# Kernel optimization log

Hardware: AMD Instinct MI355X
Metric: run time of the kernel (lower is better)

## Reference

```python
import jax, jax.numpy as jnp
import numpy as np

EMBED_DIM = 1024
NUM_HEADS = 16
HEAD_DIM = EMBED_DIM // NUM_HEADS


def setup_inputs() -> dict:
    key = jax.random.key(0)
    ks = jax.random.split(key, 9)
    B, T, C = 4, 2048, EMBED_DIM
    s = 1.0 / np.sqrt(C)
    return {
        "x": jax.random.normal(ks[0], (B, T, C), jnp.float32),
        "Wq": jax.random.normal(ks[1], (C, C), jnp.float32) * s,
        "bq": jnp.zeros((C,), jnp.float32),
        "Wk": jax.random.normal(ks[2], (C, C), jnp.float32) * s,
        "bk": jnp.zeros((C,), jnp.float32),
        "Wv": jax.random.normal(ks[3], (C, C), jnp.float32) * s,
        "bv": jnp.zeros((C,), jnp.float32),
        "Wo": jax.random.normal(ks[4], (C, C), jnp.float32) * s,
        "bo": jnp.zeros((C,), jnp.float32),
    }


def reference(x, Wq, bq, Wk, bk, Wv, bv, Wo, bo):
    B, T, C = x.shape
    H, D = NUM_HEADS, HEAD_DIM
    # projections (torch Linear: y = x @ W.T + b; here weights stored as [in, out])
    q = (x @ Wq + bq).reshape(B, T, H, D).transpose(0, 2, 1, 3)  # [B,H,T,D]
    k = (x @ Wk + bk).reshape(B, T, H, D).transpose(0, 2, 1, 3)
    v = (x @ Wv + bv).reshape(B, T, H, D).transpose(0, 2, 1, 3)
    scores = jnp.einsum("bhqd,bhkd->bhqk", q, k) / jnp.sqrt(jnp.float32(D))
    causal = jnp.tril(jnp.ones((T, T), bool))
    scores = jnp.where(causal, scores, -jnp.inf)
    attn = jax.nn.softmax(scores, axis=-1)
    out = jnp.einsum("bhqk,bhkd->bhqd", attn, v)  # [B,H,T,D]
    out = out.transpose(0, 2, 1, 3).reshape(B, T, C)
    return out @ Wo + bo
```

## Files before the change

kernel.cpp:

```cpp
#include <hip/hip_runtime.h>
#include <hip/hip_bf16.h>
#include <math.h>

typedef __hip_bfloat16 bf16_t;
typedef __attribute__((ext_vector_type(8))) short short8;
typedef __attribute__((ext_vector_type(4))) float floatx4;

#define T_SEQ 2048
#define NB    4
#define NH    16
#define HD    64
#define C_DIM 1024
#define M_ROWS (NB * T_SEQ)

#define Q_SCALE 0.18033688011f

__device__ __forceinline__ void load_lds16(const bf16_t* g, bf16_t* l) {
    __builtin_amdgcn_global_load_lds(
        (const __attribute__((address_space(1))) void*)g,
        (__attribute__((address_space(3))) void*)l,
        16, 0, 0);
}

__device__ __forceinline__ floatx4 mfma16(short8 a, short8 b, floatx4 c) {
    return __builtin_amdgcn_mfma_f32_16x16x32_bf16(a, b, c, 0, 0, 0);
}

__global__ void convert_x_kernel(const float* __restrict__ x, bf16_t* __restrict__ xb) {
    int i = blockIdx.x * 256 + threadIdx.x;
    float4 v = reinterpret_cast<const float4*>(x)[i];
    union { bf16_t h[4]; short4 s4; } u;
    u.h[0] = __float2bfloat16(v.x);
    u.h[1] = __float2bfloat16(v.y);
    u.h[2] = __float2bfloat16(v.z);
    u.h[3] = __float2bfloat16(v.w);
    reinterpret_cast<short4*>(xb)[i] = u.s4;
}

__global__ void transpose_cvt_kernel(const float* __restrict__ W0, const float* __restrict__ W1,
                                     const float* __restrict__ W2, const float* __restrict__ W3,
                                     bf16_t* __restrict__ O0, bf16_t* __restrict__ O1,
                                     bf16_t* __restrict__ O2, bf16_t* __restrict__ O3) {
    const float* W = (blockIdx.z == 0) ? W0 : (blockIdx.z == 1) ? W1 : (blockIdx.z == 2) ? W2 : W3;
    bf16_t*      O = (blockIdx.z == 0) ? O0 : (blockIdx.z == 1) ? O1 : (blockIdx.z == 2) ? O2 : O3;
    __shared__ float tile[32][33];
    int bx = blockIdx.x * 32, by = blockIdx.y * 32;
    int tx = threadIdx.x, ty = threadIdx.y;
#pragma unroll
    for (int j = 0; j < 32; j += 8)
        tile[ty + j][tx] = W[(size_t)(by + ty + j) * C_DIM + bx + tx];
    __syncthreads();
#pragma unroll
    for (int j = 0; j < 32; j += 8)
        O[(size_t)(bx + ty + j) * C_DIM + by + tx] = __float2bfloat16(tile[tx][ty + j]);
}

__device__ __forceinline__ void gemm_mainloop(const bf16_t* __restrict__ Ablk,
                                              const bf16_t* __restrict__ Bblk,
                                              bf16_t* As, bf16_t* Bs,
                                              floatx4 acc[4][4], int wave, int lane) {
    int lr = lane & 15, lq = lane >> 4;
    int wr = (wave >> 1) * 64, wc = (wave & 1) * 64;
    for (int kt = 0; kt < C_DIM; kt += 64) {
#pragma unroll
        for (int j = 0; j < 4; ++j) {
            int chunk = j * 256 + wave * 64 + lane;
            int r = chunk >> 3, ps = chunk & 7;
            int c = ((ps ^ (r & 7)) * 8);
            load_lds16(Ablk + (size_t)r * C_DIM + kt + c, As + chunk * 8);
            load_lds16(Bblk + (size_t)r * C_DIM + kt + c, Bs + chunk * 8);
        }
        __syncthreads();
#pragma unroll
        for (int kk = 0; kk < 2; ++kk) {
            short8 af[4], bfr[4];
            int psw = ((kk * 4 + lq) ^ (lr & 7)) * 8;
#pragma unroll
            for (int m = 0; m < 4; ++m)
                af[m] = *reinterpret_cast<const short8*>(As + (wr + m * 16 + lr) * 64 + psw);
#pragma unroll
            for (int n = 0; n < 4; ++n)
                bfr[n] = *reinterpret_cast<const short8*>(Bs + (wc + n * 16 + lr) * 64 + psw);
#pragma unroll
            for (int m = 0; m < 4; ++m)
#pragma unroll
                for (int n = 0; n < 4; ++n)
                    acc[m][n] = mfma16(af[m], bfr[n], acc[m][n]);
        }
        __syncthreads();
    }
}

__global__ __launch_bounds__(256, 3) void gemm_qkv_kernel(
    const bf16_t* __restrict__ xb,
    const bf16_t* __restrict__ WqT, const bf16_t* __restrict__ WkT, const bf16_t* __restrict__ WvT,
    const float* __restrict__ bq, const float* __restrict__ bk, const float* __restrict__ bv,
    bf16_t* __restrict__ Q, bf16_t* __restrict__ K, bf16_t* __restrict__ Vt) {
    __shared__ bf16_t As[128 * 64];
    __shared__ bf16_t Bs[128 * 64];
    int tid = threadIdx.x, wave = tid >> 6, lane = tid & 63;

    int f    = (int)blockIdx.x + ((int)blockIdx.y << 3) + ((int)blockIdx.z << 9);
    int xcd  = f & 7;
    int s    = f >> 3;
    int rloc = s & 7;
    int t2   = s >> 3;
    int colp = t2 & 7;
    int wsel = t2 >> 3;
    int row0 = (xcd * 8 + rloc) * 128;
    int col0 = colp * 128;

    const bf16_t* Wt  = (wsel == 0) ? WqT : (wsel == 1) ? WkT : WvT;
    const float* bias = (wsel == 0) ? bq : (wsel == 1) ? bk : bv;

    floatx4 acc[4][4] = {};
    gemm_mainloop(xb + (size_t)row0 * C_DIM, Wt + (size_t)col0 * C_DIM, As, Bs, acc, wave, lane);

    int lr = lane & 15, lq = lane >> 4;
    int wr = (wave >> 1) * 64, wc = (wave & 1) * 64;

    if (wsel == 2) {
#pragma unroll
        for (int nt = 0; nt < 4; ++nt) {
            int col = col0 + wc + nt * 16 + lr;
            float bvv = bias[col];
            int h = col >> 6, d = col & 63;
#pragma unroll
            for (int m = 0; m < 4; ++m) {
                int rowg0 = row0 + wr + m * 16 + lq * 4;
                int b = rowg0 >> 11, t0 = rowg0 & (T_SEQ - 1);
                union { bf16_t h4[4]; short4 s4; } u;
#pragma unroll
                for (int r = 0; r < 4; ++r)
                    u.h4[r] = __float2bfloat16(acc[m][nt][r] + bvv);
                *reinterpret_cast<short4*>(
                    &Vt[((size_t)((b * NH + h) * HD + d)) * T_SEQ + t0]) = u.s4;
            }
        }
    } else {
        float scale = (wsel == 0) ? Q_SCALE : 1.0f;
        bf16_t* outp = (wsel == 0) ? Q : K;
#pragma unroll
        for (int nt = 0; nt < 4; ++nt) {
            int col = col0 + wc + nt * 16 + lr;
            float bvv = bias[col];
            int h = col >> 6, d = col & 63;
#pragma unroll
            for (int m = 0; m < 4; ++m) {
#pragma unroll
                for (int r = 0; r < 4; ++r) {
                    int rowg = row0 + wr + m * 16 + lq * 4 + r;
                    int b = rowg >> 11, t = rowg & (T_SEQ - 1);
                    float val = (acc[m][nt][r] + bvv) * scale;
                    outp[((size_t)((b * NH + h) * T_SEQ + t)) * HD + d] =
                        __float2bfloat16(val);
                }
            }
        }
    }
}

__global__ __launch_bounds__(512, 4) void attn_kernel(
    const bf16_t* __restrict__ Q, const bf16_t* __restrict__ K,
    const bf16_t* __restrict__ Vt, bf16_t* __restrict__ ctx) {
    __shared__ __align__(16) bf16_t Ks[2][64 * 64];
    __shared__ __align__(16) bf16_t Vs[2][64 * 64];
    __shared__ __align__(16) unsigned short Ps[128 * 64];
    int tid = threadIdx.x, w = tid >> 6, lane = tid & 63;
    int lr = lane & 15, lq = lane >> 4;
    int xcd = (int)blockIdx.x;
    int y   = (int)blockIdx.y;
    int bh  = xcd * 8 + (y & 7);
    int qp  = y >> 3;
    int b = bh >> 4, h = bh & 15;

    const bf16_t* Kbase = K  + (size_t)bh * T_SEQ * HD;
    const bf16_t* Vbase = Vt + (size_t)bh * HD * T_SEQ;

#pragma unroll 1
    for (int pass = 0; pass < 2; ++pass) {
        int qt = pass ? qp : (15 - qp);
        int q0 = qt * 128;
        int ktiles = 2 * qt + 2;
        const bf16_t* Qbase = Q + ((size_t)bh * T_SEQ + q0) * HD;

        {
            int ch = tid;
            int r = ch >> 3, ps = ch & 7;
            int c = ((ps ^ (r & 7)) * 8);
            load_lds16(Kbase + (size_t)r * HD + c, Ks[0] + ch * 8);
            load_lds16(Vbase + (size_t)r * T_SEQ + c, Vs[0] + ch * 8);
        }

        short8 qf[2];
#pragma unroll
        for (int kk = 0; kk < 2; ++kk)
            qf[kk] = *reinterpret_cast<const short8*>(
                Qbase + (size_t)(w * 16 + lr) * HD + kk * 32 + lq * 8);

        floatx4 o[4] = {};
        float lpart[4] = {};
        int buf = 0;

        for (int it = 0; it < ktiles; ++it) {
            int kt0 = it * 64;
            __syncthreads();

            if (it + 1 < ktiles) {
                int nk0 = kt0 + 64;
                int ch = tid;
                int r = ch >> 3, ps = ch & 7;
                int c = ((ps ^ (r & 7)) * 8);
                load_lds16(Kbase + (size_t)(nk0 + r) * HD + c, Ks[buf ^ 1] + ch * 8);
                load_lds16(Vbase + (size_t)r * T_SEQ + nk0 + c, Vs[buf ^ 1] + ch * 8);
            }

            const bf16_t* Kc = Ks[buf];
            const bf16_t* Vc = Vs[buf];

            floatx4 s[4] = {};
            short8 kf[4][2];
#pragma unroll
            for (int kk = 0; kk < 2; ++kk) {
                int psw = ((kk * 4 + lq) ^ (lr & 7)) * 8;
#pragma unroll
                for (int n = 0; n < 4; ++n)
                    kf[n][kk] = *reinterpret_cast<const short8*>(Kc + (n * 16 + lr) * 64 + psw);
            }
#pragma unroll
            for (int kk = 0; kk < 2; ++kk)
#pragma unroll
                for (int n = 0; n < 4; ++n)
                    s[n] = mfma16(qf[kk], kf[n][kk], s[n]);

            if (it >= ktiles - 2) {
#pragma unroll
                for (int r = 0; r < 4; ++r) {
                    int rowg = q0 + w * 16 + lq * 4 + r;
#pragma unroll
                    for (int n = 0; n < 4; ++n) {
                        int colg = kt0 + n * 16 + lr;
                        if (colg > rowg) s[n][r] = -1e30f;
                    }
                }
            }

#pragma unroll
            for (int n = 0; n < 4; ++n)
#pragma unroll
                for (int r = 0; r < 4; ++r)
                    s[n][r] = __builtin_amdgcn_exp2f(s[n][r]);
#pragma unroll
            for (int r = 0; r < 4; ++r)
                lpart[r] += (s[0][r] + s[1][r]) + (s[2][r] + s[3][r]);

#pragma unroll
            for (int n = 0; n < 4; ++n)
#pragma unroll
                for (int r = 0; r < 4; ++r) {
                    int prow = w * 16 + lq * 4 + r;
                    int piece = n * 2 + (lr >> 3);
                    union { float f; unsigned u; } cv; cv.f = s[n][r];
                    Ps[prow * 64 + ((piece ^ (prow & 7)) * 8) + (lr & 7)] =
                        (unsigned short)(cv.u >> 16);
                }

            short8 pf[2], vf[4][2];
#pragma unroll
            for (int kk = 0; kk < 2; ++kk) {
                int prow = w * 16 + lr;
                pf[kk] = *reinterpret_cast<const short8*>(
                    Ps + prow * 64 + (((kk * 4 + lq) ^ (lr & 7)) * 8));
            }
#pragma unroll
            for (int kk = 0; kk < 2; ++kk) {
                int psw = ((kk * 4 + lq) ^ (lr & 7)) * 8;
#pragma unroll
                for (int dt = 0; dt < 4; ++dt)
                    vf[dt][kk] = *reinterpret_cast<const short8*>(Vc + (dt * 16 + lr) * 64 + psw);
            }
#pragma unroll
            for (int kk = 0; kk < 2; ++kk)
#pragma unroll
                for (int dt = 0; dt < 4; ++dt)
                    o[dt] = mfma16(pf[kk], vf[dt][kk], o[dt]);

            buf ^= 1;
        }

#pragma unroll
        for (int r = 0; r < 4; ++r) {
            float l = lpart[r];
            l += __shfl_xor(l, 1);
            l += __shfl_xor(l, 2);
            l += __shfl_xor(l, 4);
            l += __shfl_xor(l, 8);
            float inv = 1.0f / l;
            int t = q0 + w * 16 + lq * 4 + r;
#pragma unroll
            for (int dt = 0; dt < 4; ++dt) {
                int d = dt * 16 + lr;
                ctx[((size_t)(b * T_SEQ + t)) * C_DIM + h * HD + d] =
                    __float2bfloat16(o[dt][r] * inv);
            }
        }
    }
}

__global__ __launch_bounds__(256, 3) void gemm_out_kernel(
    const bf16_t* __restrict__ Actx, const bf16_t* __restrict__ WoT,
    const float* __restrict__ bo, float* __restrict__ out) {
    __shared__ bf16_t As[128 * 64];
    __shared__ bf16_t Bs[128 * 64];
    int tid = threadIdx.x, wave = tid >> 6, lane = tid & 63;

    int f    = (int)blockIdx.x + ((int)blockIdx.y << 3);
    int xcd  = f & 7;
    int s    = f >> 3;
    int rloc = s & 7;
    int colp = s >> 3;
    int row0 = (xcd * 8 + rloc) * 128;
    int col0 = colp * 128;

    floatx4 acc[4][4] = {};
    gemm_mainloop(Actx + (size_t)row0 * C_DIM, WoT + (size_t)col0 * C_DIM, As, Bs, acc, wave, lane);
    int lr = lane & 15, lq = lane >> 4;
    int wr = (wave >> 1) * 64, wc = (wave & 1) * 64;
#pragma unroll
    for (int nt = 0; nt < 4; ++nt) {
        int col = col0 + wc + nt * 16 + lr;
        float bvv = bo[col];
#pragma unroll
        for (int m = 0; m < 4; ++m)
#pragma unroll
            for (int r = 0; r < 4; ++r) {
                int rowg = row0 + wr + m * 16 + lq * 4 + r;
                out[(size_t)rowg * C_DIM + col] = acc[m][nt][r] + bvv;
            }
    }
}

extern "C" void kernel_launch(void* const* d_in, const int* in_sizes, int n_in,
                              void* d_out, int out_size, void* d_ws, size_t ws_size,
                              hipStream_t stream) {
    const float* x  = (const float*)d_in[0];
    const float* Wq = (const float*)d_in[1];
    const float* bq = (const float*)d_in[2];
    const float* Wk = (const float*)d_in[3];
    const float* bk = (const float*)d_in[4];
    const float* Wv = (const float*)d_in[5];
    const float* bv = (const float*)d_in[6];
    const float* Wo = (const float*)d_in[7];
    const float* bo = (const float*)d_in[8];
    float* out = (float*)d_out;

    char* ws = (char*)d_ws;
    bf16_t* xb  = (bf16_t*)ws; ws += (size_t)M_ROWS * C_DIM * 2;
    bf16_t* WqT = (bf16_t*)ws; ws += (size_t)C_DIM * C_DIM * 2;
    bf16_t* WkT = (bf16_t*)ws; ws += (size_t)C_DIM * C_DIM * 2;
    bf16_t* WvT = (bf16_t*)ws; ws += (size_t)C_DIM * C_DIM * 2;
    bf16_t* WoT = (bf16_t*)ws; ws += (size_t)C_DIM * C_DIM * 2;
    bf16_t* Qb  = (bf16_t*)ws; ws += (size_t)M_ROWS * C_DIM * 2;
    bf16_t* Kb  = (bf16_t*)ws; ws += (size_t)M_ROWS * C_DIM * 2;
    bf16_t* Vtb = (bf16_t*)ws; ws += (size_t)M_ROWS * C_DIM * 2;
    bf16_t* ctx = (bf16_t*)ws; ws += (size_t)M_ROWS * C_DIM * 2;

    convert_x_kernel<<<(M_ROWS * C_DIM / 4) / 256, 256, 0, stream>>>(x, xb);
    transpose_cvt_kernel<<<dim3(32, 32, 4), dim3(32, 8), 0, stream>>>(
        Wq, Wk, Wv, Wo, WqT, WkT, WvT, WoT);
    gemm_qkv_kernel<<<dim3(8, 64, 3), 256, 0, stream>>>(
        xb, WqT, WkT, WvT, bq, bk, bv, Qb, Kb, Vtb);
    attn_kernel<<<dim3(8, 64), 512, 0, stream>>>(Qb, Kb, Vtb, ctx);
    gemm_out_kernel<<<dim3(8, 64), 256, 0, stream>>>(ctx, WoT, bo, out);
}
```

Before: 245.4 us.

## Software-pipeline attention loop: defer PV matmul by one tile with triple-buffered K/V

Restructures the attention inner loop so the P·V MFMA for the previous tile is issued alongside the QK^T MFMA of the current tile. K/V shared buffers become triple-buffered and P is double-buffered, so the P write in one iteration is read in the next, after the barrier. This removes the write-then-read dependency on P within an iteration and gives more independent MFMA work per barrier. The cost is more LDS (3 K/V tiles plus 2 P tiles), which may reduce occupancy at 4 blocks per CU, and more live registers.

```diff
diff --git a/kernel.cpp b/kernel.cpp
--- a/kernel.cpp
+++ b/kernel.cpp
@@ -160,12 +160,103 @@
     }
 }
 
+__device__ __forceinline__ void attn_iter(
+    int it, int ktiles, int q0, int tid, int w, int lr, int lq,
+    const bf16_t* __restrict__ Kbase, const bf16_t* __restrict__ Vbase,
+    bf16_t* KsC, bf16_t* VsC, bf16_t* KsN, bf16_t* VsN, const bf16_t* VsP,
+    unsigned short* PsW, const unsigned short* PsR,
+    const short8 qf[2], floatx4 o[4], float lpart[4], bool do_pv)
+{
+    int kt0 = it * 64;
+    __syncthreads();
+
+    if (it + 1 < ktiles) {
+        int nk0 = kt0 + 64;
+        int ch = tid;
+        int r = ch >> 3, ps = ch & 7;
+        int c = ((ps ^ (r & 7)) * 8);
+        load_lds16(Kbase + (size_t)(nk0 + r) * HD + c, KsN + ch * 8);
+        load_lds16(Vbase + (size_t)r * T_SEQ + nk0 + c, VsN + ch * 8);
+    }
+
+    short8 pf[2], vp[4][2];
+    if (do_pv) {
+        int prow = w * 16 + lr;
+#pragma unroll
+        for (int kk = 0; kk < 2; ++kk)
+            pf[kk] = *reinterpret_cast<const short8*>(
+                PsR + prow * 64 + (((kk * 4 + lq) ^ (lr & 7)) * 8));
+#pragma unroll
+        for (int kk = 0; kk < 2; ++kk) {
+            int psw = ((kk * 4 + lq) ^ (lr & 7)) * 8;
+#pragma unroll
+            for (int dt = 0; dt < 4; ++dt)
+                vp[dt][kk] = *reinterpret_cast<const short8*>(VsP + (dt * 16 + lr) * 64 + psw);
+        }
+    }
+    short8 kf[4][2];
+#pragma unroll
+    for (int kk = 0; kk < 2; ++kk) {
+        int psw = ((kk * 4 + lq) ^ (lr & 7)) * 8;
+#pragma unroll
+        for (int n = 0; n < 4; ++n)
+            kf[n][kk] = *reinterpret_cast<const short8*>(KsC + (n * 16 + lr) * 64 + psw);
+    }
+
+    if (do_pv) {
+#pragma unroll
+        for (int kk = 0; kk < 2; ++kk)
+#pragma unroll
+            for (int dt = 0; dt < 4; ++dt)
+                o[dt] = mfma16(pf[kk], vp[dt][kk], o[dt]);
+    }
+
+    floatx4 s[4] = {};
+#pragma unroll
+    for (int kk = 0; kk < 2; ++kk)
+#pragma unroll
+        for (int n = 0; n < 4; ++n)
+            s[n] = mfma16(qf[kk], kf[n][kk], s[n]);
+
+    if (it >= ktiles - 2) {
+#pragma unroll
+        for (int r = 0; r < 4; ++r) {
+            int rowg = q0 + w * 16 + lq * 4 + r;
+#pragma unroll
+            for (int n = 0; n < 4; ++n) {
+                int colg = kt0 + n * 16 + lr;
+                if (colg > rowg) s[n][r] = -1e30f;
+            }
+        }
+    }
+
+#pragma unroll
+    for (int n = 0; n < 4; ++n)
+#pragma unroll
+        for (int r = 0; r < 4; ++r)
+            s[n][r] = __builtin_amdgcn_exp2f(s[n][r]);
+#pragma unroll
+    for (int r = 0; r < 4; ++r)
+        lpart[r] += (s[0][r] + s[1][r]) + (s[2][r] + s[3][r]);
+
+#pragma unroll
+    for (int n = 0; n < 4; ++n)
+#pragma unroll
+        for (int r = 0; r < 4; ++r) {
+            int prow = w * 16 + lq * 4 + r;
+            int piece = n * 2 + (lr >> 3);
+            union { float f; unsigned u; } cv; cv.f = s[n][r];
+            PsW[prow * 64 + ((piece ^ (prow & 7)) * 8) + (lr & 7)] =
+                (unsigned short)(cv.u >> 16);
+        }
+}
+
 __global__ __launch_bounds__(512, 4) void attn_kernel(
     const bf16_t* __restrict__ Q, const bf16_t* __restrict__ K,
     const bf16_t* __restrict__ Vt, bf16_t* __restrict__ ctx) {
-    __shared__ __align__(16) bf16_t Ks[2][64 * 64];
-    __shared__ __align__(16) bf16_t Vs[2][64 * 64];
-    __shared__ __align__(16) unsigned short Ps[128 * 64];
+    __shared__ __align__(16) bf16_t Ks0[64 * 64], Ks1[64 * 64], Ks2[64 * 64];
+    __shared__ __align__(16) bf16_t Vs0[64 * 64], Vs1[64 * 64], Vs2[64 * 64];
+    __shared__ __align__(16) unsigned short Ps0[128 * 64], Ps1[128 * 64];
     int tid = threadIdx.x, w = tid >> 6, lane = tid & 63;
     int lr = lane & 15, lq = lane >> 4;
     int xcd = (int)blockIdx.x;
@@ -188,8 +279,8 @@
             int ch = tid;
             int r = ch >> 3, ps = ch & 7;
             int c = ((ps ^ (r & 7)) * 8);
-            load_lds16(Kbase + (size_t)r * HD + c, Ks[0] + ch * 8);
-            load_lds16(Vbase + (size_t)r * T_SEQ + c, Vs[0] + ch * 8);
+            load_lds16(Kbase + (size_t)r * HD + c, Ks0 + ch * 8);
+            load_lds16(Vbase + (size_t)r * T_SEQ + c, Vs0 + ch * 8);
         }
 
         short8 qf[2];
@@ -200,93 +291,42 @@
 
         floatx4 o[4] = {};
         float lpart[4] = {};
-        int buf = 0;
-
-        for (int it = 0; it < ktiles; ++it) {
-            int kt0 = it * 64;
-            __syncthreads();
-
-            if (it + 1 < ktiles) {
-                int nk0 = kt0 + 64;
-                int ch = tid;
-                int r = ch >> 3, ps = ch & 7;
-                int c = ((ps ^ (r & 7)) * 8);
-                load_lds16(Kbase + (size_t)(nk0 + r) * HD + c, Ks[buf ^ 1] + ch * 8);
-                load_lds16(Vbase + (size_t)r * T_SEQ + nk0 + c, Vs[buf ^ 1] + ch * 8);
-            }
-
-            const bf16_t* Kc = Ks[buf];
-            const bf16_t* Vc = Vs[buf];
-
-            floatx4 s[4] = {};
-            short8 kf[4][2];
+
+        bf16_t *KsC = Ks0, *KsN = Ks1, *KsP = Ks2;
+        bf16_t *VsC = Vs0, *VsN = Vs1, *VsP = Vs2;
+
+        for (int it2 = 0; it2 < ktiles; it2 += 2) {
+            attn_iter(it2, ktiles, q0, tid, w, lr, lq, Kbase, Vbase,
+                      KsC, VsC, KsN, VsN, VsP, Ps0, Ps1, qf, o, lpart, it2 > 0);
+            { bf16_t* t = KsC; KsC = KsN; KsN = KsP; KsP = t; }
+            { bf16_t* t = VsC; VsC = VsN; VsN = VsP; VsP = t; }
+            attn_iter(it2 + 1, ktiles, q0, tid, w, lr, lq, Kbase, Vbase,
+                      KsC, VsC, KsN, VsN, VsP, Ps1, Ps0, qf, o, lpart, true);
+            { bf16_t* t = KsC; KsC = KsN; KsN = KsP; KsP = t; }
+            { bf16_t* t = VsC; VsC = VsN; VsN = VsP; VsP = t; }
+        }
+
+        {
+            int prow = w * 16 + lr;
+            short8 pf[2], vp[4][2];
+#pragma unroll
+            for (int kk = 0; kk < 2; ++kk)
+                pf[kk] = *reinterpret_cast<const short8*>(
+                    Ps1 + prow * 64 + (((kk * 4 + lq) ^ (lr & 7)) * 8));
 #pragma unroll
             for (int kk = 0; kk < 2; ++kk) {
                 int psw = ((kk * 4 + lq) ^ (lr & 7)) * 8;
 #pragma unroll
-                for (int n = 0; n < 4; ++n)
-                    kf[n][kk] = *reinterpret_cast<const short8*>(Kc + (n * 16 + lr) * 64 + psw);
+                for (int dt = 0; dt < 4; ++dt)
+                    vp[dt][kk] = *reinterpret_cast<const short8*>(VsP + (dt * 16 + lr) * 64 + psw);
             }
 #pragma unroll
             for (int kk = 0; kk < 2; ++kk)
 #pragma unroll
-                for (int n = 0; n < 4; ++n)
-                    s[n] = mfma16(qf[kk], kf[n][kk], s[n]);
-
-            if (it >= ktiles - 2) {
-#pragma unroll
-                for (int r = 0; r < 4; ++r) {
-                    int rowg = q0 + w * 16 + lq * 4 + r;
-#pragma unroll
-                    for (int n = 0; n < 4; ++n) {
-                        int colg = kt0 + n * 16 + lr;
-                        if (colg > rowg) s[n][r] = -1e30f;
-                    }
-                }
-            }
-
-#pragma unroll
-            for (int n = 0; n < 4; ++n)
-#pragma unroll
-                for (int r = 0; r < 4; ++r)
-                    s[n][r] = __builtin_amdgcn_exp2f(s[n][r]);
-#pragma unroll
-            for (int r = 0; r < 4; ++r)
-                lpart[r] += (s[0][r] + s[1][r]) + (s[2][r] + s[3][r]);
-
-#pragma unroll
-            for (int n = 0; n < 4; ++n)
-#pragma unroll
-                for (int r = 0; r < 4; ++r) {
-                    int prow = w * 16 + lq * 4 + r;
-                    int piece = n * 2 + (lr >> 3);
-                    union { float f; unsigned u; } cv; cv.f = s[n][r];
-                    Ps[prow * 64 + ((piece ^ (prow & 7)) * 8) + (lr & 7)] =
-                        (unsigned short)(cv.u >> 16);
-                }
-
-            short8 pf[2], vf[4][2];
-#pragma unroll
-            for (int kk = 0; kk < 2; ++kk) {
-                int prow = w * 16 + lr;
-                pf[kk] = *reinterpret_cast<const short8*>(
-                    Ps + prow * 64 + (((kk * 4 + lq) ^ (lr & 7)) * 8));
-            }
-#pragma unroll
-            for (int kk = 0; kk < 2; ++kk) {
-                int psw = ((kk * 4 + lq) ^ (lr & 7)) * 8;
-#pragma unroll
                 for (int dt = 0; dt < 4; ++dt)
-                    vf[dt][kk] = *reinterpret_cast<const short8*>(Vc + (dt * 16 + lr) * 64 + psw);
-            }
-#pragma unroll
-            for (int kk = 0; kk < 2; ++kk)
-#pragma unroll
-                for (int dt = 0; dt < 4; ++dt)
-                    o[dt] = mfma16(pf[kk], vf[dt][kk], o[dt]);
-
-            buf ^= 1;
-        }
+                    o[dt] = mfma16(pf[kk], vp[dt][kk], o[dt]);
+        }
+        __syncthreads();
 
 #pragma unroll
         for (int r = 0; r < 4; ++r) {
```

Result: slower. 266.7 us (+8.7%).
